# Optimization experiments

Hardware: AMD Instinct MI355X
Metric: run time of the kernel (lower is better)

The kernel has to match this reference:

```python
import jax, jax.numpy as jnp
import numpy as np

MAX_ITER = 6
M_HIST = 2
BETA = 0.9
LAM = 1e-4


def setup_inputs() -> dict:
    key = jax.random.key(0)
    k1, k2, k3, k4 = jax.random.split(key, 4)
    B, D = 1024, 2048
    x = jax.random.normal(k1, (B, D), dtype=jnp.float32)
    # small init scale keeps the fixed-point map contractive-ish
    Wz = jax.random.normal(k2, (D, D), dtype=jnp.float32) * 0.02
    Wx = jax.random.normal(k3, (D, D), dtype=jnp.float32) * 0.02
    b = jax.random.normal(k4, (D,), dtype=jnp.float32) * 0.02
    return {"x": x, "Wz": Wz, "Wx": Wx, "b": b}


def _anderson_solve(f, z_init):
    """Faithful port of anderson_acceleration_fixed (fixed iteration count)."""
    batch_size = z_init.shape[0]
    d = z_init.size // batch_size
    dtype = z_init.dtype

    def step_fn(i, state):
        z, G_hist, Z_hist, min_residual = state
        f_z = f(z)
        g = f_z - z
        residual = jnp.linalg.norm(g.reshape(batch_size, -1), axis=-1)
        min_residual = jnp.minimum(min_residual, residual)
        z_flat = z.reshape(batch_size, -1)
        g_flat = g.reshape(batch_size, -1)
        G_hist = jnp.roll(G_hist, 1, axis=1).at[:, 0, :].set(g_flat)
        Z_hist = jnp.roll(Z_hist, 1, axis=1).at[:, 0, :].set(z_flat)

        def simple_update(_):
            return (z_flat + BETA * g_flat).astype(dtype)

        def anderson_update(_):
            current_g = G_hist[:, 0, :]
            current_z = Z_hist[:, 0, :]
            # only the first history difference is used (matches source)
            DG_0 = (current_g - G_hist[:, 1, :]).astype(jnp.float32)
            DZ_0 = (current_z - Z_hist[:, 1, :]).astype(jnp.float32)
            cg = current_g.astype(jnp.float32)
            zf = z_flat.astype(jnp.float32)
            numerator = jnp.sum(DG_0 * cg, axis=-1)
            denominator = jnp.sum(DG_0 * DG_0, axis=-1) + LAM
            gamma = numerator / denominator
            correction = gamma[:, None] * (DZ_0 + BETA * DG_0)
            return (zf + BETA * cg - correction).astype(dtype)

        z_new_flat = jax.lax.cond(i < M_HIST, simple_update, anderson_update, None)
        return (z_new_flat.reshape(z.shape), G_hist, Z_hist, min_residual)

    G_hist = jnp.zeros((batch_size, M_HIST, d), dtype=dtype)
    Z_hist = jnp.zeros((batch_size, M_HIST, d), dtype=dtype)
    min_residual = jnp.full((batch_size,), 1e6, dtype=jnp.float32)
    z_star, _, _, _ = jax.lax.fori_loop(
        0, MAX_ITER, step_fn, (z_init, G_hist, Z_hist, min_residual))
    return z_star


def reference(x, Wz, Wx, b):
    # DEQ block: f(z, x) = tanh(z @ Wz + x @ Wx + b)
    x_proj = x @ Wx + b  # injection, constant across iterations

    def f(z):
        return jnp.tanh(z @ Wz + x_proj)

    z_init = jnp.zeros_like(x)
    z_star = _anderson_solve(f, z_init)
    return z_star
```

## Files before the change

kernel.cpp:

```cpp
#include <hip/hip_runtime.h>
#include <stdint.h>

#define MDIM 1024
#define NDIM 2048
#define KDIM 2048
#define BETAC 0.9f
#define LAMC 1e-4f

typedef __attribute__((ext_vector_type(4))) float f32x4;
typedef __attribute__((ext_vector_type(8))) short s16x8;

typedef __attribute__((address_space(3))) unsigned int as3_u32;
typedef __attribute__((address_space(1))) unsigned int as1_u32;

__device__ __forceinline__ void gload_lds16(const void* g, const void* l) {
  __builtin_amdgcn_global_load_lds((const as1_u32*)(uintptr_t)g,
                                   (as3_u32*)(unsigned int)(uintptr_t)l, 16, 0, 0);
}

__device__ __forceinline__ unsigned short f2bf(float f) {
  union { float f; unsigned u; } x; x.f = f;
  unsigned r = x.u + 0x7fffu + ((x.u >> 16) & 1u);
  return (unsigned short)(r >> 16);
}

__global__ __launch_bounds__(256) void transpose_cvt2_kernel(const float* __restrict__ Wz,
                                                             const float* __restrict__ Wx,
                                                             unsigned short* __restrict__ WzT,
                                                             unsigned short* __restrict__ WxT) {
  const float* W = blockIdx.z ? Wx : Wz;
  unsigned short* WT = blockIdx.z ? WxT : WzT;
  __shared__ float tile[32][33];
  const int tx = threadIdx.x, ty = threadIdx.y;
  const int col = blockIdx.x * 32 + tx;
  const int row0 = blockIdx.y * 32 + ty;
#pragma unroll
  for (int j = 0; j < 32; j += 8)
    tile[ty + j][tx] = W[(size_t)(row0 + j) * NDIM + col];
  __syncthreads();
  const int ocol = blockIdx.y * 32 + tx;
  const int orow0 = blockIdx.x * 32 + ty;
#pragma unroll
  for (int j = 0; j < 32; j += 8)
    WT[(size_t)(orow0 + j) * KDIM + ocol] = f2bf(tile[tx][ty + j]);
}

__global__ __launch_bounds__(256) void cvt_bf16_kernel(const float* __restrict__ in,
                                                       unsigned short* __restrict__ out, int n4) {
  int i = blockIdx.x * blockDim.x + threadIdx.x;
  if (i >= n4) return;
  f32x4 v = ((const f32x4*)in)[i];
  ushort4 o;
  o.x = f2bf(v[0]); o.y = f2bf(v[1]); o.z = f2bf(v[2]); o.w = f2bf(v[3]);
  ((ushort4*)out)[i] = o;
}

__global__ __launch_bounds__(256) void gemm_split_kernel(const unsigned short* __restrict__ A,
                                                         const unsigned short* __restrict__ BT,
                                                         float* __restrict__ P0,
                                                         float* __restrict__ P1) {
  __shared__ short As[2][64 * 64];
  __shared__ short Bs[2][128 * 64];

  const int tid = threadIdx.x;
  const int l = tid & 63;
  const int w = tid >> 6;
  const int wr = w >> 1, wc = w & 1;
  const int row0 = blockIdx.y * 64;
  const int col0 = blockIdx.x * 128;
  const int kbase = blockIdx.z * (KDIM / 2);
  const int lrow = l & 15;
  const int lk8 = (l >> 4) * 8;
  const int wuni = (tid & ~63) * 8;

  f32x4 acc[2][4];
#pragma unroll
  for (int mi = 0; mi < 2; mi++)
#pragma unroll
    for (int ni = 0; ni < 4; ni++) acc[mi][ni] = f32x4{0.f, 0.f, 0.f, 0.f};

  auto stage = [&](int k0, int buf) {
#pragma unroll
    for (int p = 0; p < 2; p++) {
      int u = p * 256 + tid;
      int r = u >> 3;
      int c = ((u & 7) ^ (r & 7)) * 8;
      const unsigned short* src = A + (size_t)(row0 + r) * KDIM + k0 + c;
      const short* dst = &As[buf][p * 2048 + wuni];
      gload_lds16(src, dst);
    }
#pragma unroll
    for (int p = 0; p < 4; p++) {
      int u = p * 256 + tid;
      int r = u >> 3;
      int c = ((u & 7) ^ (r & 7)) * 8;
      const unsigned short* src = BT + (size_t)(col0 + r) * KDIM + k0 + c;
      const short* dst = &Bs[buf][p * 2048 + wuni];
      gload_lds16(src, dst);
    }
  };

  constexpr int NT = (KDIM / 2) / 64;
  stage(kbase, 0);
  asm volatile("s_waitcnt vmcnt(0)" ::: "memory");
  __syncthreads();

  for (int t = 0; t < NT; ++t) {
    const int cur = t & 1;
    if (t + 1 < NT) stage(kbase + (t + 1) * 64, cur ^ 1);
#pragma unroll
    for (int ks = 0; ks < 2; ++ks) {
      const int kk = ks * 32 + lk8;
      s16x8 a[2], b[4];
#pragma unroll
      for (int mi = 0; mi < 2; mi++) {
        int rr = wr * 32 + mi * 16 + lrow;
        int sidx = (rr * 64 + kk) ^ ((rr & 7) << 3);
        a[mi] = *(const s16x8*)(&As[cur][sidx]);
      }
#pragma unroll
      for (int ni = 0; ni < 4; ni++) {
        int rr = wc * 64 + ni * 16 + lrow;
        int sidx = (rr * 64 + kk) ^ ((rr & 7) << 3);
        b[ni] = *(const s16x8*)(&Bs[cur][sidx]);
      }
#pragma unroll
      for (int mi = 0; mi < 2; mi++)
#pragma unroll
        for (int ni = 0; ni < 4; ni++)
          acc[mi][ni] = __builtin_amdgcn_mfma_f32_16x16x32_bf16(a[mi], b[ni], acc[mi][ni], 0, 0, 0);
    }
    asm volatile("s_waitcnt vmcnt(0)" ::: "memory");
    __syncthreads();
  }

  float* __restrict__ P = blockIdx.z ? P1 : P0;
#pragma unroll
  for (int mi = 0; mi < 2; mi++) {
#pragma unroll
    for (int ni = 0; ni < 4; ni++) {
      const int col = col0 + wc * 64 + ni * 16 + lrow;
      const int rbase = row0 + wr * 32 + mi * 16 + (l >> 4) * 4;
#pragma unroll
      for (int j = 0; j < 4; j++)
        P[(size_t)(rbase + j) * NDIM + col] = acc[mi][ni][j];
    }
  }
}

template <int MODE>
__global__ __launch_bounds__(256) void rowfused_kernel(const float* __restrict__ P0,
                                                       const float* __restrict__ P1,
                                                       const float* __restrict__ xp_or_bias,
                                                       const float* __restrict__ z,
                                                       const float* __restrict__ zp,
                                                       const float* __restrict__ gp,
                                                       float* __restrict__ gout,
                                                       float* __restrict__ zout,
                                                       unsigned short* __restrict__ zbout,
                                                       float* __restrict__ xpout) {
  const int row = blockIdx.x;
  const int tid = threadIdx.x;
  const size_t b4 = (size_t)row * (NDIM / 4);
  __shared__ float sn[4], sd[4];
  __shared__ float sga;

  int vi[2] = {tid, tid + 256};
  f32x4 gv[2], znv[2], zv[2], zpv[2], gpv[2];
  float num = 0.f, den = 0.f;

#pragma unroll
  for (int h = 0; h < 2; h++) {
    const size_t q = b4 + vi[h];
    f32x4 p0 = ((const f32x4*)P0)[q];
    f32x4 p1 = ((const f32x4*)P1)[q];
    f32x4 xb;
    if (MODE == 0) xb = ((const f32x4*)xp_or_bias)[vi[h]];
    else xb = ((const f32x4*)xp_or_bias)[q];
    if (MODE != 0) zv[h] = ((const f32x4*)z)[q];
    if (MODE >= 2) {
      zpv[h] = ((const f32x4*)zp)[q];
      gpv[h] = ((const f32x4*)gp)[q];
    }
#pragma unroll
    for (int j = 0; j < 4; j++) {
      const float s = p0[j] + p1[j] + xb[j];
      if (MODE == 0) {
        const float z1 = BETAC * tanhf(s);
        gv[h][j] = s;
        znv[h][j] = z1;
      } else {
        const float g = tanhf(s) - zv[h][j];
        gv[h][j] = g;
        if (MODE == 1) znv[h][j] = zv[h][j] + BETAC * g;
        else {
          const float dg = g - gpv[h][j];
          num += dg * g;
          den += dg * dg;
        }
      }
    }
  }

  if (MODE >= 2) {
#pragma unroll
    for (int off = 32; off > 0; off >>= 1) {
      num += __shfl_down(num, off);
      den += __shfl_down(den, off);
    }
    if ((tid & 63) == 0) { sn[tid >> 6] = num; sd[tid >> 6] = den; }
    __syncthreads();
    if (tid == 0)
      sga = (sn[0] + sn[1] + sn[2] + sn[3]) / (sd[0] + sd[1] + sd[2] + sd[3] + LAMC);
    __syncthreads();
    const float ga = sga;
#pragma unroll
    for (int h = 0; h < 2; h++)
#pragma unroll
      for (int j = 0; j < 4; j++)
        znv[h][j] = zv[h][j] + BETAC * gv[h][j]
                  - ga * ((zv[h][j] - zpv[h][j]) + BETAC * (gv[h][j] - gpv[h][j]));
  }

#pragma unroll
  for (int h = 0; h < 2; h++) {
    const size_t q = b4 + vi[h];
    if (MODE == 0) ((f32x4*)xpout)[q] = gv[h];
    if (MODE == 1 || MODE == 2) ((f32x4*)gout)[q] = gv[h];
    ((f32x4*)zout)[q] = znv[h];
    if (MODE != 3) {
      ushort4 o;
      o.x = f2bf(znv[h][0]); o.y = f2bf(znv[h][1]);
      o.z = f2bf(znv[h][2]); o.w = f2bf(znv[h][3]);
      ((ushort4*)zbout)[q] = o;
    }
  }
}

extern "C" void kernel_launch(void* const* d_in, const int* in_sizes, int n_in,
                              void* d_out, int out_size, void* d_ws, size_t ws_size,
                              hipStream_t stream) {
  const float* x = (const float*)d_in[0];
  const float* Wz = (const float*)d_in[1];
  const float* Wx = (const float*)d_in[2];
  const float* bias = (const float*)d_in[3];

  const size_t MN = (size_t)MDIM * NDIM;
  const size_t KN = (size_t)KDIM * NDIM;
  char* ws = (char*)d_ws;
  size_t off = 0;
  auto alloc = [&](size_t bytes) -> void* {
    void* p = ws + off;
    off += (bytes + 255) & ~(size_t)255;
    return p;
  };
  unsigned short* WzT = (unsigned short*)alloc(KN * 2);
  unsigned short* WxT = (unsigned short*)alloc(KN * 2);
  unsigned short* xb = (unsigned short*)alloc(MN * 2);
  float* xproj = (float*)alloc(MN * 4);
  float* zA = (float*)alloc(MN * 4);
  float* zB = (float*)alloc(MN * 4);
  float* gA = (float*)alloc(MN * 4);
  float* gB = (float*)alloc(MN * 4);
  unsigned short* zb16 = (unsigned short*)alloc(MN * 2);
  float* P0 = (float*)alloc(MN * 4);
  float* P1 = (float*)alloc(MN * 4);
  (void)ws_size;

  const int n4 = (int)(MN / 4);
  const dim3 tb(32, 8);
  const dim3 tgrid(NDIM / 32, KDIM / 32, 2);
  const dim3 ggrid(NDIM / 128, MDIM / 64, 2);
  const int ewblocks = n4 / 256;

  transpose_cvt2_kernel<<<tgrid, tb, 0, stream>>>(Wz, Wx, WzT, WxT);
  cvt_bf16_kernel<<<ewblocks, 256, 0, stream>>>(x, xb, n4);

  gemm_split_kernel<<<ggrid, 256, 0, stream>>>(xb, WxT, P0, P1);
  rowfused_kernel<0><<<MDIM, 256, 0, stream>>>(P0, P1, bias, nullptr, nullptr, nullptr,
                                               nullptr, zA, zb16, xproj);

  float* zc = zA;
  float* zp = zB;
  float* gc = gA;
  float* gp = gB;

  gemm_split_kernel<<<ggrid, 256, 0, stream>>>(zb16, WzT, P0, P1);
  rowfused_kernel<1><<<MDIM, 256, 0, stream>>>(P0, P1, xproj, zc, nullptr, nullptr,
                                               gc, zp, zb16, nullptr);
  { float* t = zc; zc = zp; zp = t; }
  { float* t = gc; gc = gp; gp = t; }

  for (int it = 2; it < 5; ++it) {
    gemm_split_kernel<<<ggrid, 256, 0, stream>>>(zb16, WzT, P0, P1);
    rowfused_kernel<2><<<MDIM, 256, 0, stream>>>(P0, P1, xproj, zc, zp, gp,
                                                 gc, zp, zb16, nullptr);
    { float* t = zc; zc = zp; zp = t; }
    { float* t = gc; gc = gp; gp = t; }
  }

  gemm_split_kernel<<<ggrid, 256, 0, stream>>>(zb16, WzT, P0, P1);
  rowfused_kernel<3><<<MDIM, 256, 0, stream>>>(P0, P1, xproj, zc, zp, gp,
                                               nullptr, (float*)d_out, nullptr, nullptr);
}
```

Baseline: 169.4 us.

## Use 128x128 GEMM tiles with triple-buffered LDS prefetch and fuse prep kernels

The split-K GEMM block grows from 64x128 to 128x128 output with 512 threads (8 waves). LDS goes from double to triple buffering with a two-stage-ahead prefetch and partial vmcnt waits, and MFMA sections are raised in priority with s_setprio. The x-to-bf16 conversion is folded into the weight transpose kernel as an extra grid slice, which saves one launch. The aim is more reuse per tile and better hiding of load latency. The cost is fewer blocks (256 total) on a 256-CU part and more LDS per block (96KB).

After: 173.1 us. 1.02x slower.

```diff
diff --git a/kernel.cpp b/kernel.cpp
--- a/kernel.cpp
+++ b/kernel.cpp
@@ -24,10 +24,24 @@
   return (unsigned short)(r >> 16);
 }
 
-__global__ __launch_bounds__(256) void transpose_cvt2_kernel(const float* __restrict__ Wz,
-                                                             const float* __restrict__ Wx,
-                                                             unsigned short* __restrict__ WzT,
-                                                             unsigned short* __restrict__ WxT) {
+__global__ __launch_bounds__(256) void prep_kernel(const float* __restrict__ Wz,
+                                                   const float* __restrict__ Wx,
+                                                   unsigned short* __restrict__ WzT,
+                                                   unsigned short* __restrict__ WxT,
+                                                   const float* __restrict__ x,
+                                                   unsigned short* __restrict__ xb) {
+  if (blockIdx.z == 2) {
+    const int b = blockIdx.y * 64 + blockIdx.x;
+    const int t = threadIdx.y * 32 + threadIdx.x;
+    if (t < 128) {
+      const int i = b * 128 + t;
+      f32x4 v = ((const f32x4*)x)[i];
+      ushort4 o;
+      o.x = f2bf(v[0]); o.y = f2bf(v[1]); o.z = f2bf(v[2]); o.w = f2bf(v[3]);
+      ((ushort4*)xb)[i] = o;
+    }
+    return;
+  }
   const float* W = blockIdx.z ? Wx : Wz;
   unsigned short* WT = blockIdx.z ? WxT : WzT;
   __shared__ float tile[32][33];
@@ -45,28 +59,19 @@
     WT[(size_t)(orow0 + j) * KDIM + ocol] = f2bf(tile[tx][ty + j]);
 }
 
-__global__ __launch_bounds__(256) void cvt_bf16_kernel(const float* __restrict__ in,
-                                                       unsigned short* __restrict__ out, int n4) {
-  int i = blockIdx.x * blockDim.x + threadIdx.x;
-  if (i >= n4) return;
-  f32x4 v = ((const f32x4*)in)[i];
-  ushort4 o;
-  o.x = f2bf(v[0]); o.y = f2bf(v[1]); o.z = f2bf(v[2]); o.w = f2bf(v[3]);
-  ((ushort4*)out)[i] = o;
-}
-
-__global__ __launch_bounds__(256) void gemm_split_kernel(const unsigned short* __restrict__ A,
+__global__ __launch_bounds__(512) void gemm_split_kernel(const unsigned short* __restrict__ A,
                                                          const unsigned short* __restrict__ BT,
                                                          float* __restrict__ P0,
                                                          float* __restrict__ P1) {
-  __shared__ short As[2][64 * 64];
-  __shared__ short Bs[2][128 * 64];
+  __shared__ short As[3][128 * 64];
+  __shared__ short Bs[3][128 * 64];
 
   const int tid = threadIdx.x;
   const int l = tid & 63;
   const int w = tid >> 6;
-  const int wr = w >> 1, wc = w & 1;
-  const int row0 = blockIdx.y * 64;
+  const int wr = w >> 1;
+  const int wc = w & 1;
+  const int row0 = blockIdx.y * 128;
   const int col0 = blockIdx.x * 128;
   const int kbase = blockIdx.z * (KDIM / 2);
   const int lrow = l & 15;
@@ -82,32 +87,33 @@
   auto stage = [&](int k0, int buf) {
 #pragma unroll
     for (int p = 0; p < 2; p++) {
-      int u = p * 256 + tid;
+      int u = p * 512 + tid;
       int r = u >> 3;
       int c = ((u & 7) ^ (r & 7)) * 8;
-      const unsigned short* src = A + (size_t)(row0 + r) * KDIM + k0 + c;
-      const short* dst = &As[buf][p * 2048 + wuni];
-      gload_lds16(src, dst);
-    }
-#pragma unroll
-    for (int p = 0; p < 4; p++) {
-      int u = p * 256 + tid;
+      gload_lds16(A + (size_t)(row0 + r) * KDIM + k0 + c, &As[buf][p * 4096 + wuni]);
+    }
+#pragma unroll
+    for (int p = 0; p < 2; p++) {
+      int u = p * 512 + tid;
       int r = u >> 3;
       int c = ((u & 7) ^ (r & 7)) * 8;
-      const unsigned short* src = BT + (size_t)(col0 + r) * KDIM + k0 + c;
-      const short* dst = &Bs[buf][p * 2048 + wuni];
-      gload_lds16(src, dst);
+      gload_lds16(BT + (size_t)(col0 + r) * KDIM + k0 + c, &Bs[buf][p * 4096 + wuni]);
     }
   };
 
   constexpr int NT = (KDIM / 2) / 64;
   stage(kbase, 0);
-  asm volatile("s_waitcnt vmcnt(0)" ::: "memory");
+  stage(kbase + 64, 1);
+  asm volatile("s_waitcnt vmcnt(4)" ::: "memory");
   __syncthreads();
 
+  int cur = 0;
   for (int t = 0; t < NT; ++t) {
-    const int cur = t & 1;
-    if (t + 1 < NT) stage(kbase + (t + 1) * 64, cur ^ 1);
+    const int sb = (cur == 0) ? 2 : (cur - 1);
+    if (t + 2 < NT) stage(kbase + (t + 2) * 64, sb);
+
+    const short* __restrict__ Acur = As[cur];
+    const short* __restrict__ Bcur = Bs[cur];
 #pragma unroll
     for (int ks = 0; ks < 2; ++ks) {
       const int kk = ks * 32 + lk8;
@@ -116,22 +122,30 @@
       for (int mi = 0; mi < 2; mi++) {
         int rr = wr * 32 + mi * 16 + lrow;
         int sidx = (rr * 64 + kk) ^ ((rr & 7) << 3);
-        a[mi] = *(const s16x8*)(&As[cur][sidx]);
+        a[mi] = *(const s16x8*)(&Acur[sidx]);
       }
 #pragma unroll
       for (int ni = 0; ni < 4; ni++) {
         int rr = wc * 64 + ni * 16 + lrow;
         int sidx = (rr * 64 + kk) ^ ((rr & 7) << 3);
-        b[ni] = *(const s16x8*)(&Bs[cur][sidx]);
+        b[ni] = *(const s16x8*)(&Bcur[sidx]);
       }
+      __builtin_amdgcn_s_setprio(1);
 #pragma unroll
       for (int mi = 0; mi < 2; mi++)
 #pragma unroll
         for (int ni = 0; ni < 4; ni++)
           acc[mi][ni] = __builtin_amdgcn_mfma_f32_16x16x32_bf16(a[mi], b[ni], acc[mi][ni], 0, 0, 0);
-    }
-    asm volatile("s_waitcnt vmcnt(0)" ::: "memory");
+      __builtin_amdgcn_s_setprio(0);
+    }
+
+    if (t + 2 < NT) {
+      asm volatile("s_waitcnt vmcnt(4)" ::: "memory");
+    } else {
+      asm volatile("s_waitcnt vmcnt(0)" ::: "memory");
+    }
     __syncthreads();
+    cur = (cur == 2) ? 0 : (cur + 1);
   }
 
   float* __restrict__ P = blockIdx.z ? P1 : P0;
@@ -267,16 +281,13 @@
   float* P1 = (float*)alloc(MN * 4);
   (void)ws_size;
 
-  const int n4 = (int)(MN / 4);
   const dim3 tb(32, 8);
-  const dim3 tgrid(NDIM / 32, KDIM / 32, 2);
-  const dim3 ggrid(NDIM / 128, MDIM / 64, 2);
-  const int ewblocks = n4 / 256;
-
-  transpose_cvt2_kernel<<<tgrid, tb, 0, stream>>>(Wz, Wx, WzT, WxT);
-  cvt_bf16_kernel<<<ewblocks, 256, 0, stream>>>(x, xb, n4);
-
-  gemm_split_kernel<<<ggrid, 256, 0, stream>>>(xb, WxT, P0, P1);
+  const dim3 pgrid(NDIM / 32, KDIM / 32, 3);
+  const dim3 ggrid(NDIM / 128, MDIM / 128, 2);
+
+  prep_kernel<<<pgrid, tb, 0, stream>>>(Wz, Wx, WzT, WxT, x, xb);
+
+  gemm_split_kernel<<<ggrid, 512, 0, stream>>>(xb, WxT, P0, P1);
   rowfused_kernel<0><<<MDIM, 256, 0, stream>>>(P0, P1, bias, nullptr, nullptr, nullptr,
                                                nullptr, zA, zb16, xproj);
 
@@ -285,21 +296,21 @@
   float* gc = gA;
   float* gp = gB;
 
-  gemm_split_kernel<<<ggrid, 256, 0, stream>>>(zb16, WzT, P0, P1);
+  gemm_split_kernel<<<ggrid, 512, 0, stream>>>(zb16, WzT, P0, P1);
   rowfused_kernel<1><<<MDIM, 256, 0, stream>>>(P0, P1, xproj, zc, nullptr, nullptr,
                                                gc, zp, zb16, nullptr);
   { float* t = zc; zc = zp; zp = t; }
   { float* t = gc; gc = gp; gp = t; }
 
   for (int it = 2; it < 5; ++it) {
-    gemm_split_kernel<<<ggrid, 256, 0, stream>>>(zb16, WzT, P0, P1);
+    gemm_split_kernel<<<ggrid, 512, 0, stream>>>(zb16, WzT, P0, P1);
     rowfused_kernel<2><<<MDIM, 256, 0, stream>>>(P0, P1, xproj, zc, zp, gp,
                                                  gc, zp, zb16, nullptr);
     { float* t = zc; zc = zp; zp = t; }
     { float* t = gc; gc = gp; gp = t; }
   }
 
-  gemm_split_kernel<<<ggrid, 256, 0, stream>>>(zb16, WzT, P0, P1);
+  gemm_split_kernel<<<ggrid, 512, 0, stream>>>(zb16, WzT, P0, P1);
   rowfused_kernel<3><<<MDIM, 256, 0, stream>>>(P0, P1, xproj, zc, zp, gp,
                                                nullptr, (float*)d_out, nullptr, nullptr);
 }
```

## Remap GEMM blocks per XCD, merge prep kernels, raise MFMA wave priority

Applied to the files above, without the earlier changes.

The GEMM grid becomes a flat 512-block launch. Each block's tile index is rebuilt from its XCD id (bid&7), so that the k-splits and a group of M rows for the same N tiles sit on the same XCD and share L2 reuse of A and B. The x-to-bf16 conversion is folded into the weight transpose kernel as an extra grid slice, which removes one launch. s_setprio is raised around the MFMA block to favour waves that are issuing matrix work. The remapping assumes round-robin dispatch of blocks to the eight XCDs.

Result: faster. 163.4 us (-3.5%).

```diff
diff --git a/kernel.cpp b/kernel.cpp
--- a/kernel.cpp
+++ b/kernel.cpp
@@ -24,10 +24,24 @@
   return (unsigned short)(r >> 16);
 }
 
-__global__ __launch_bounds__(256) void transpose_cvt2_kernel(const float* __restrict__ Wz,
-                                                             const float* __restrict__ Wx,
-                                                             unsigned short* __restrict__ WzT,
-                                                             unsigned short* __restrict__ WxT) {
+__global__ __launch_bounds__(256) void prep_kernel(const float* __restrict__ Wz,
+                                                   const float* __restrict__ Wx,
+                                                   unsigned short* __restrict__ WzT,
+                                                   unsigned short* __restrict__ WxT,
+                                                   const float* __restrict__ x,
+                                                   unsigned short* __restrict__ xb) {
+  if (blockIdx.z == 2) {
+    const int b = blockIdx.y * 64 + blockIdx.x;
+    const int t = threadIdx.y * 32 + threadIdx.x;
+    if (t < 128) {
+      const int i = b * 128 + t;
+      f32x4 v = ((const f32x4*)x)[i];
+      ushort4 o;
+      o.x = f2bf(v[0]); o.y = f2bf(v[1]); o.z = f2bf(v[2]); o.w = f2bf(v[3]);
+      ((ushort4*)xb)[i] = o;
+    }
+    return;
+  }
   const float* W = blockIdx.z ? Wx : Wz;
   unsigned short* WT = blockIdx.z ? WxT : WzT;
   __shared__ float tile[32][33];
@@ -45,16 +59,6 @@
     WT[(size_t)(orow0 + j) * KDIM + ocol] = f2bf(tile[tx][ty + j]);
 }
 
-__global__ __launch_bounds__(256) void cvt_bf16_kernel(const float* __restrict__ in,
-                                                       unsigned short* __restrict__ out, int n4) {
-  int i = blockIdx.x * blockDim.x + threadIdx.x;
-  if (i >= n4) return;
-  f32x4 v = ((const f32x4*)in)[i];
-  ushort4 o;
-  o.x = f2bf(v[0]); o.y = f2bf(v[1]); o.z = f2bf(v[2]); o.w = f2bf(v[3]);
-  ((ushort4*)out)[i] = o;
-}
-
 __global__ __launch_bounds__(256) void gemm_split_kernel(const unsigned short* __restrict__ A,
                                                          const unsigned short* __restrict__ BT,
                                                          float* __restrict__ P0,
@@ -62,13 +66,20 @@
   __shared__ short As[2][64 * 64];
   __shared__ short Bs[2][128 * 64];
 
+  const int bid = blockIdx.x;
+  const int xcd = bid & 7;
+  const int slot = bid >> 3;
+  const int nb = slot & 15;
+  const int mb = (xcd >> 1) * 4 + (slot >> 4);
+  const int ksplit = xcd & 1;
+
   const int tid = threadIdx.x;
   const int l = tid & 63;
   const int w = tid >> 6;
   const int wr = w >> 1, wc = w & 1;
-  const int row0 = blockIdx.y * 64;
-  const int col0 = blockIdx.x * 128;
-  const int kbase = blockIdx.z * (KDIM / 2);
+  const int row0 = mb * 64;
+  const int col0 = nb * 128;
+  const int kbase = ksplit * (KDIM / 2);
   const int lrow = l & 15;
   const int lk8 = (l >> 4) * 8;
   const int wuni = (tid & ~63) * 8;
@@ -85,18 +96,14 @@
       int u = p * 256 + tid;
       int r = u >> 3;
       int c = ((u & 7) ^ (r & 7)) * 8;
-      const unsigned short* src = A + (size_t)(row0 + r) * KDIM + k0 + c;
-      const short* dst = &As[buf][p * 2048 + wuni];
-      gload_lds16(src, dst);
+      gload_lds16(A + (size_t)(row0 + r) * KDIM + k0 + c, &As[buf][p * 2048 + wuni]);
     }
 #pragma unroll
     for (int p = 0; p < 4; p++) {
       int u = p * 256 + tid;
       int r = u >> 3;
       int c = ((u & 7) ^ (r & 7)) * 8;
-      const unsigned short* src = BT + (size_t)(col0 + r) * KDIM + k0 + c;
-      const short* dst = &Bs[buf][p * 2048 + wuni];
-      gload_lds16(src, dst);
+      gload_lds16(BT + (size_t)(col0 + r) * KDIM + k0 + c, &Bs[buf][p * 2048 + wuni]);
     }
   };
 
@@ -124,17 +131,19 @@
         int sidx = (rr * 64 + kk) ^ ((rr & 7) << 3);
         b[ni] = *(const s16x8*)(&Bs[cur][sidx]);
       }
+      __builtin_amdgcn_s_setprio(1);
 #pragma unroll
       for (int mi = 0; mi < 2; mi++)
 #pragma unroll
         for (int ni = 0; ni < 4; ni++)
           acc[mi][ni] = __builtin_amdgcn_mfma_f32_16x16x32_bf16(a[mi], b[ni], acc[mi][ni], 0, 0, 0);
+      __builtin_amdgcn_s_setprio(0);
     }
     asm volatile("s_waitcnt vmcnt(0)" ::: "memory");
     __syncthreads();
   }
 
-  float* __restrict__ P = blockIdx.z ? P1 : P0;
+  float* __restrict__ P = ksplit ? P1 : P0;
 #pragma unroll
   for (int mi = 0; mi < 2; mi++) {
 #pragma unroll
@@ -267,14 +276,11 @@
   float* P1 = (float*)alloc(MN * 4);
   (void)ws_size;
 
-  const int n4 = (int)(MN / 4);
   const dim3 tb(32, 8);
-  const dim3 tgrid(NDIM / 32, KDIM / 32, 2);
-  const dim3 ggrid(NDIM / 128, MDIM / 64, 2);
-  const int ewblocks = n4 / 256;
-
-  transpose_cvt2_kernel<<<tgrid, tb, 0, stream>>>(Wz, Wx, WzT, WxT);
-  cvt_bf16_kernel<<<ewblocks, 256, 0, stream>>>(x, xb, n4);
+  const dim3 pgrid(NDIM / 32, KDIM / 32, 3);
+  const int ggrid = 512;
+
+  prep_kernel<<<pgrid, tb, 0, stream>>>(Wz, Wx, WzT, WxT, x, xb);
 
   gemm_split_kernel<<<ggrid, 256, 0, stream>>>(xb, WxT, P0, P1);
   rowfused_kernel<0><<<MDIM, 256, 0, stream>>>(P0, P1, bias, nullptr, nullptr, nullptr,
```
